# Performance work log

Hardware: AMD Instinct MI355X
Metric: run time of the kernel (lower is better)

The kernel has to match this reference:

```python
import jax, jax.numpy as jnp
import numpy as np

H = 8      # num_attention_heads
DH = 96    # attention_head_size
LN_EPS = 1e-5


def setup_inputs() -> dict:
    key = jax.random.key(0)
    ks = jax.random.split(key, 12)
    B, S, D = 2, 768, 768
    sc = 0.02
    return {
        "hidden_states": jax.random.normal(ks[0], (B, S, D), jnp.float32),
        "distance_matrix": jax.random.uniform(ks[1], (B, S, S), jnp.float32) * 20.0,
        "angle_matrix": jax.random.uniform(ks[2], (B, S, S), jnp.float32) * np.pi,
        "attention_mask": jnp.ones((B, S), jnp.float32),
        "Wq": jax.random.normal(ks[3], (D, D), jnp.float32) * sc,
        "bq": jnp.zeros((D,), jnp.float32),
        "Wk": jax.random.normal(ks[4], (D, D), jnp.float32) * sc,
        "bk": jnp.zeros((D,), jnp.float32),
        "Wv": jax.random.normal(ks[5], (D, D), jnp.float32) * sc,
        "bv": jnp.zeros((D,), jnp.float32),
        "Wd": jax.random.normal(ks[6], (DH,), jnp.float32) * sc,
        "bd": jnp.zeros((DH,), jnp.float32),
        "Wa": jax.random.normal(ks[7], (DH,), jnp.float32) * sc,
        "ba": jnp.zeros((DH,), jnp.float32),
        "Wo": jax.random.normal(ks[8], (D, D), jnp.float32) * sc,
        "bo": jnp.zeros((D,), jnp.float32),
        "ln_g": jnp.ones((D,), jnp.float32),
        "ln_b": jnp.zeros((D,), jnp.float32),
    }


def _heads(x, B, S):
    # [B,S,D] -> [B,H,S,DH]
    return x.reshape(B, S, H, DH).transpose(0, 2, 1, 3)


def reference(hidden_states, distance_matrix, angle_matrix, attention_mask,
              Wq, bq, Wk, bk, Wv, bv, Wd, bd, Wa, ba, Wo, bo, ln_g, ln_b):
    B, S, D = hidden_states.shape
    q = _heads(hidden_states @ Wq.T + bq, B, S)   # [B,H,S,DH]
    k = _heads(hidden_states @ Wk.T + bk, B, S)
    v = _heads(hidden_states @ Wv.T + bv, B, S)

    scores = jnp.einsum('bhid,bhjd->bhij', q, k) / jnp.sqrt(jnp.float32(DH))

    # distance / angle relative-position biases: emb[b,i,j,:] = dist[b,i,j]*Wd + bd
    dist_emb = distance_matrix[..., None] * Wd + bd   # [B,S,S,DH]
    scores = scores + jnp.einsum('bhid,bijd->bhij', q, dist_emb)
    ang_emb = angle_matrix[..., None] * Wa + ba       # [B,S,S,DH]
    scores = scores + jnp.einsum('bhid,bijd->bhij', q, ang_emb)

    # key mask, broadcast over heads and query positions
    scores = scores + (1.0 - attention_mask)[:, None, None, :] * -10000.0

    probs = jax.nn.softmax(scores, axis=-1)           # [B,H,S,S]
    ctx = jnp.einsum('bhij,bhjd->bhid', probs, v)
    ctx = ctx.transpose(0, 2, 1, 3).reshape(B, S, D)  # [B,S,D]

    out = ctx @ Wo.T + bo
    x = out + hidden_states
    mu = jnp.mean(x, axis=-1, keepdims=True)
    var = jnp.var(x, axis=-1, keepdims=True)
    out = (x - mu) * jax.lax.rsqrt(var + LN_EPS) * ln_g + ln_b
    return out, probs
```

## Files before the change

### kernel.cpp

```cpp
#include <hip/hip_runtime.h>
#include <stdint.h>

#define B_  2
#define S_  768
#define D_  768
#define H_  8
#define DH_ 96

typedef unsigned short ushort_t;
typedef __bf16 bf16x8 __attribute__((ext_vector_type(8)));
typedef float  f32x4  __attribute__((ext_vector_type(4)));

__device__ inline ushort_t f2bf(float f) {
    union { float f; unsigned int u; } v; v.f = f;
    unsigned int u = v.u;
    unsigned int r = u + 0x7fffu + ((u >> 16) & 1u);
    return (ushort_t)(r >> 16);
}
__device__ inline float bf2f(ushort_t u) {
    union { unsigned int i; float f; } c; c.i = ((unsigned int)u) << 16;
    return c.f;
}

__device__ inline void glds16(const void* gp, void* lp) {
    auto g = reinterpret_cast<const __attribute__((address_space(1))) uint32_t*>(
        reinterpret_cast<uintptr_t>(gp));
    auto l = reinterpret_cast<__attribute__((address_space(3))) uint32_t*>(
        reinterpret_cast<uintptr_t>(lp));
    __builtin_amdgcn_global_load_lds(g, l, 16, 0, 0);
}

__global__ __launch_bounds__(256) void k_convert(
        const float* __restrict__ X, const float* __restrict__ Wq,
        const float* __restrict__ Wk, const float* __restrict__ Wv,
        const float* __restrict__ Wo,
        ushort_t* __restrict__ Xb, ushort_t* __restrict__ Wb) {
    const int NX4 = (B_ * S_ * D_) / 4;
    const int NW4 = (D_ * D_) / 4;
    int i = blockIdx.x * blockDim.x + threadIdx.x;
    float4 v;
    ushort_t* dst;
    if (i < NX4) {
        v = ((const float4*)X)[i];
        dst = Xb + i * 4;
    } else {
        int wi = i - NX4;
        int sel = wi / NW4;
        int off = wi - sel * NW4;
        const float* src = (sel == 0) ? Wq : (sel == 1) ? Wk : (sel == 2) ? Wv : Wo;
        v = ((const float4*)src)[off];
        dst = Wb + wi * 4;
    }
    ushort4 o;
    o.x = f2bf(v.x); o.y = f2bf(v.y); o.z = f2bf(v.z); o.w = f2bf(v.w);
    *(ushort4*)dst = o;
}

__device__ inline void gemm64_glds(
        const ushort_t* __restrict__ A, int lda,
        const ushort_t* __restrict__ Bt, int ldb,
        int K, int m0, int n0,
        ushort_t* As, ushort_t* Bs, f32x4 acc[2][2]) {
    const int tid  = threadIdx.x;
    const int lane = tid & 63, wave = tid >> 6;
    const int wm = (wave >> 1) * 32, wn = (wave & 1) * 32;
    const int fr = lane & 15, fk = (lane >> 4) * 8;
    const int sr = wave * 16 + (lane >> 2);
    const int sc = (lane & 3) * 8;
    const ushort_t* Ap = A  + (size_t)(m0 + sr) * lda + sc;
    const ushort_t* Bp = Bt + (size_t)(n0 + sr) * ldb + sc;
    ushort_t* AsW = As + wave * 512;
    ushort_t* BsW = Bs + wave * 512;
    for (int kt = 0; kt < K; kt += 32) {
        if (kt) __syncthreads();
        glds16(Ap + kt, AsW);
        glds16(Bp + kt, BsW);
        __syncthreads();
        bf16x8 a0 = *(const bf16x8*)&As[(wm      + fr) * 32 + fk];
        bf16x8 a1 = *(const bf16x8*)&As[(wm + 16 + fr) * 32 + fk];
        bf16x8 b0 = *(const bf16x8*)&Bs[(wn      + fr) * 32 + fk];
        bf16x8 b1 = *(const bf16x8*)&Bs[(wn + 16 + fr) * 32 + fk];
        acc[0][0] = __builtin_amdgcn_mfma_f32_16x16x32_bf16(a0, b0, acc[0][0], 0, 0, 0);
        acc[0][1] = __builtin_amdgcn_mfma_f32_16x16x32_bf16(a0, b1, acc[0][1], 0, 0, 0);
        acc[1][0] = __builtin_amdgcn_mfma_f32_16x16x32_bf16(a1, b0, acc[1][0], 0, 0, 0);
        acc[1][1] = __builtin_amdgcn_mfma_f32_16x16x32_bf16(a1, b1, acc[1][1], 0, 0, 0);
    }
}

__global__ __launch_bounds__(256) void k_qkv(
        const ushort_t* __restrict__ Xb, const ushort_t* __restrict__ Wb,
        const float* __restrict__ bq, const float* __restrict__ bk,
        const float* __restrict__ bv,
        ushort_t* __restrict__ Qb, ushort_t* __restrict__ Kb,
        ushort_t* __restrict__ Vtb) {
    __shared__ __align__(16) ushort_t As[128 * 32];
    __shared__ __align__(16) ushort_t Bs[64 * 32];
    f32x4 acc[4][2];
    #pragma unroll
    for (int i = 0; i < 4; i++)
        #pragma unroll
        for (int j = 0; j < 2; j++) acc[i][j] = (f32x4){0.f, 0.f, 0.f, 0.f};
    const int tid = threadIdx.x, lane = tid & 63, wave = tid >> 6;
    const int m0 = blockIdx.y * 128, n0 = blockIdx.x * 64;
    const int fr = lane & 15, fk = (lane >> 4) * 8;
    const int wm = (wave >> 1) * 64, wn = (wave & 1) * 32;
    const int sr = lane >> 2, sc = (lane & 3) * 8;
    const ushort_t* Ap0 = Xb + (size_t)(m0 + wave * 32 + sr) * D_ + sc;
    const ushort_t* Ap1 = Ap0 + 16 * D_;
    const ushort_t* Bp  = Wb + (size_t)(n0 + wave * 16 + sr) * D_ + sc;
    ushort_t* AsW0 = As + wave * 1024;
    ushort_t* AsW1 = As + wave * 1024 + 512;
    ushort_t* BsW  = Bs + wave * 512;
    for (int kt = 0; kt < D_; kt += 32) {
        if (kt) __syncthreads();
        glds16(Ap0 + kt, AsW0);
        glds16(Ap1 + kt, AsW1);
        glds16(Bp  + kt, BsW);
        __syncthreads();
        bf16x8 a[4], b[2];
        #pragma unroll
        for (int mi = 0; mi < 4; mi++)
            a[mi] = *(const bf16x8*)&As[(wm + mi * 16 + fr) * 32 + fk];
        #pragma unroll
        for (int ni = 0; ni < 2; ni++)
            b[ni] = *(const bf16x8*)&Bs[(wn + ni * 16 + fr) * 32 + fk];
        #pragma unroll
        for (int mi = 0; mi < 4; mi++)
            #pragma unroll
            for (int ni = 0; ni < 2; ni++)
                acc[mi][ni] = __builtin_amdgcn_mfma_f32_16x16x32_bf16(a[mi], b[ni], acc[mi][ni], 0, 0, 0);
    }
    #pragma unroll
    for (int ni = 0; ni < 2; ni++) {
        int gcol = n0 + wn + ni * 16 + fr;
        int g = gcol / D_, d768 = gcol - g * D_;
        int h = d768 / DH_, d = d768 - h * DH_;
        float bias = (g == 0 ? bq : (g == 1 ? bk : bv))[d768];
        #pragma unroll
        for (int mi = 0; mi < 4; mi++) {
            #pragma unroll
            for (int r = 0; r < 4; r++) {
                int grow = m0 + wm + mi * 16 + (lane >> 4) * 4 + r;
                int bidx = grow / S_, s = grow - bidx * S_;
                ushort_t ob = f2bf(acc[mi][ni][r] + bias);
                int bh = bidx * H_ + h;
                if (g == 0)      Qb[((size_t)bh * S_ + s) * DH_ + d] = ob;
                else if (g == 1) Kb[((size_t)bh * S_ + s) * DH_ + d] = ob;
                else             Vtb[((size_t)bh * DH_ + d) * S_ + s] = ob;
            }
        }
    }
}

__global__ __launch_bounds__(256) void k_qcoef(
        const ushort_t* __restrict__ Qb,
        const float* __restrict__ Wd, const float* __restrict__ bd,
        const float* __restrict__ Wa, const float* __restrict__ ba,
        float* __restrict__ qcoef) {
    const int wave = threadIdx.x >> 6, lane = threadIdx.x & 63;
    const int row = blockIdx.x * 4 + wave;
    const ushort_t* q = Qb + (size_t)row * DH_;
    float e0 = bf2f(q[lane]);
    float c0 = e0 * Wd[lane];
    float c1 = e0 * Wa[lane];
    float c2 = e0 * (bd[lane] + ba[lane]);
    if (lane < 32) {
        int d = 64 + lane;
        float e1 = bf2f(q[d]);
        c0 += e1 * Wd[d];
        c1 += e1 * Wa[d];
        c2 += e1 * (bd[d] + ba[d]);
    }
    #pragma unroll
    for (int o = 32; o > 0; o >>= 1) {
        c0 += __shfl_down(c0, o);
        c1 += __shfl_down(c1, o);
        c2 += __shfl_down(c2, o);
    }
    if (lane == 0) {
        qcoef[row * 3 + 0] = c0;
        qcoef[row * 3 + 1] = c1;
        qcoef[row * 3 + 2] = c2;
    }
}

__global__ __launch_bounds__(256) void k_scores(
        const ushort_t* __restrict__ Qb, const ushort_t* __restrict__ Kb,
        const float* __restrict__ qcoef,
        const float* __restrict__ distm, const float* __restrict__ angm,
        const float* __restrict__ mask, float* __restrict__ Sc) {
    __shared__ __align__(16) ushort_t As[64 * 32];
    __shared__ __align__(16) ushort_t Bs[64 * 32];
    f32x4 acc[2][2];
    #pragma unroll
    for (int i = 0; i < 2; i++)
        #pragma unroll
        for (int j = 0; j < 2; j++) acc[i][j] = (f32x4){0.f, 0.f, 0.f, 0.f};
    const int bh = blockIdx.z, b = bh >> 3;
    const ushort_t* A  = Qb + (size_t)bh * S_ * DH_;
    const ushort_t* Bt = Kb + (size_t)bh * S_ * DH_;
    const int m0 = blockIdx.y * 64, n0 = blockIdx.x * 64;
    gemm64_glds(A, DH_, Bt, DH_, DH_, m0, n0, As, Bs, acc);
    const int lane = threadIdx.x & 63, wave = threadIdx.x >> 6;
    const int wm = (wave >> 1) * 32, wn = (wave & 1) * 32;
    const float isq = 0.10206207261596577f;
    #pragma unroll
    for (int ni = 0; ni < 2; ni++) {
        int j = n0 + wn + ni * 16 + (lane & 15);
        float mb = (1.0f - mask[b * S_ + j]) * -10000.0f;
        #pragma unroll
        for (int mi = 0; mi < 2; mi++) {
            #pragma unroll
            for (int r = 0; r < 4; r++) {
                int i = m0 + wm + mi * 16 + (lane >> 4) * 4 + r;
                const float* qc = qcoef + ((size_t)bh * S_ + i) * 3;
                float dist = distm[((size_t)b * S_ + i) * S_ + j];
                float ang  = angm [((size_t)b * S_ + i) * S_ + j];
                Sc[((size_t)bh * S_ + i) * S_ + j] =
                    acc[mi][ni][r] * isq + dist * qc[0] + ang * qc[1] + qc[2] + mb;
            }
        }
    }
}

__global__ __launch_bounds__(256) void k_attnctx(
        const float* __restrict__ Sc, const ushort_t* __restrict__ Vtb,
        float* __restrict__ probs, ushort_t* __restrict__ Ctxb) {
    const int bh = blockIdx.y, b = bh >> 3, h = bh & 7;
    const int r0 = blockIdx.x * 32;
    const float* S = Sc + ((size_t)bh * S_ + r0) * S_;
    const ushort_t* Vt = Vtb + (size_t)bh * DH_ * S_;
    __shared__ float mrow[32], lrow[32];
    __shared__ __align__(16) ushort_t Ps[32 * 32];
    __shared__ __align__(16) ushort_t Vs[96 * 32];
    const int tid = threadIdx.x, lane = tid & 63, wave = tid >> 6;
    for (int rr = 0; rr < 8; rr++) {
        int row = wave * 8 + rr;
        const float* sr = S + (size_t)row * S_;
        float4 x0 = ((const float4*)sr)[lane];
        float4 x1 = ((const float4*)sr)[lane + 64];
        float4 x2 = ((const float4*)sr)[lane + 128];
        float mx = fmaxf(fmaxf(fmaxf(x0.x, x0.y), fmaxf(x0.z, x0.w)),
                   fmaxf(fmaxf(fmaxf(x1.x, x1.y), fmaxf(x1.z, x1.w)),
                         fmaxf(fmaxf(x2.x, x2.y), fmaxf(x2.z, x2.w))));
        #pragma unroll
        for (int o = 32; o > 0; o >>= 1) mx = fmaxf(mx, __shfl_down(mx, o));
        mx = __shfl(mx, 0);
        float s = __expf(x0.x - mx) + __expf(x0.y - mx) + __expf(x0.z - mx) + __expf(x0.w - mx)
                + __expf(x1.x - mx) + __expf(x1.y - mx) + __expf(x1.z - mx) + __expf(x1.w - mx)
                + __expf(x2.x - mx) + __expf(x2.y - mx) + __expf(x2.z - mx) + __expf(x2.w - mx);
        #pragma unroll
        for (int o = 32; o > 0; o >>= 1) s += __shfl_down(s, o);
        if (lane == 0) { mrow[row] = mx; lrow[row] = s; }
    }
    __syncthreads();
    const int mrow0 = (wave & 1) * 16;
    const int nb    = (wave >> 1) * 48;
    const int fr = lane & 15, fk = (lane >> 4) * 8;
    const int prow = tid >> 3, pc = (tid & 7) * 4;
    const float pm = mrow[prow];
    const float pinvl = 1.0f / lrow[prow];
    f32x4 acc[3];
    #pragma unroll
    for (int i = 0; i < 3; i++) acc[i] = (f32x4){0.f, 0.f, 0.f, 0.f};
    const int vr0 = tid >> 2, vc0 = (tid & 3) * 8;
    const int i1 = tid + 256;
    const int vr1 = i1 >> 2, vc1 = (i1 & 3) * 8;
    for (int kt = 0; kt < S_; kt += 32) {
        if (kt) __syncthreads();
        {
            float4 s4 = *(const float4*)(S + (size_t)prow * S_ + kt + pc);
            float e0 = __expf(s4.x - pm), e1 = __expf(s4.y - pm);
            float e2 = __expf(s4.z - pm), e3 = __expf(s4.w - pm);
            ushort4 pb;
            pb.x = f2bf(e0); pb.y = f2bf(e1); pb.z = f2bf(e2); pb.w = f2bf(e3);
            *(ushort4*)&Ps[prow * 32 + pc] = pb;
            float4 pn = {e0 * pinvl, e1 * pinvl, e2 * pinvl, e3 * pinvl};
            *(float4*)&probs[((size_t)bh * S_ + r0 + prow) * S_ + kt + pc] = pn;
        }
        *(uint4*)&Vs[vr0 * 32 + vc0] = *(const uint4*)(Vt + (size_t)vr0 * S_ + kt + vc0);
        if (i1 < 384)
            *(uint4*)&Vs[vr1 * 32 + vc1] = *(const uint4*)(Vt + (size_t)vr1 * S_ + kt + vc1);
        __syncthreads();
        bf16x8 a = *(const bf16x8*)&Ps[(mrow0 + fr) * 32 + fk];
        #pragma unroll
        for (int ni = 0; ni < 3; ni++) {
            bf16x8 bfr = *(const bf16x8*)&Vs[(nb + ni * 16 + fr) * 32 + fk];
            acc[ni] = __builtin_amdgcn_mfma_f32_16x16x32_bf16(a, bfr, acc[ni], 0, 0, 0);
        }
    }
    #pragma unroll
    for (int ni = 0; ni < 3; ni++) {
        int col = nb + ni * 16 + fr;
        #pragma unroll
        for (int r = 0; r < 4; r++) {
            int row = mrow0 + (lane >> 4) * 4 + r;
            float o = acc[ni][r] / lrow[row];
            Ctxb[((size_t)(b * S_ + r0 + row)) * D_ + h * DH_ + col] = f2bf(o);
        }
    }
}

__global__ __launch_bounds__(256) void k_out(
        const ushort_t* __restrict__ Ctxb, const ushort_t* __restrict__ Wob,
        const float* __restrict__ bo, const float* __restrict__ hidden,
        float* __restrict__ xbuf) {
    __shared__ __align__(16) ushort_t As[64 * 32];
    __shared__ __align__(16) ushort_t Bs[64 * 32];
    f32x4 acc[2][2];
    #pragma unroll
    for (int i = 0; i < 2; i++)
        #pragma unroll
        for (int j = 0; j < 2; j++) acc[i][j] = (f32x4){0.f, 0.f, 0.f, 0.f};
    const int m0 = blockIdx.y * 64, n0 = blockIdx.x * 64;
    gemm64_glds(Ctxb, D_, Wob, D_, D_, m0, n0, As, Bs, acc);
    const int lane = threadIdx.x & 63, wave = threadIdx.x >> 6;
    const int wm = (wave >> 1) * 32, wn = (wave & 1) * 32;
    #pragma unroll
    for (int ni = 0; ni < 2; ni++) {
        int gcol = n0 + wn + ni * 16 + (lane & 15);
        float bias = bo[gcol];
        #pragma unroll
        for (int mi = 0; mi < 2; mi++) {
            #pragma unroll
            for (int r = 0; r < 4; r++) {
                int grow = m0 + wm + mi * 16 + (lane >> 4) * 4 + r;
                xbuf[(size_t)grow * D_ + gcol] =
                    acc[mi][ni][r] + bias + hidden[(size_t)grow * D_ + gcol];
            }
        }
    }
}

__global__ __launch_bounds__(256) void k_ln(
        const float* __restrict__ xbuf, const float* __restrict__ g,
        const float* __restrict__ bb, float* __restrict__ out) {
    const float* x = xbuf + (size_t)blockIdx.x * D_;
    const int t = threadIdx.x;
    float a0 = x[t], a1 = x[t + 256], a2 = x[t + 512];
    float s = a0 + a1 + a2;
    float ss = a0 * a0 + a1 * a1 + a2 * a2;
    __shared__ float r1[4], r2[4];
    #pragma unroll
    for (int o = 32; o > 0; o >>= 1) { s += __shfl_down(s, o); ss += __shfl_down(ss, o); }
    if ((t & 63) == 0) { r1[t >> 6] = s; r2[t >> 6] = ss; }
    __syncthreads();
    float ts = r1[0] + r1[1] + r1[2] + r1[3];
    float tss = r2[0] + r2[1] + r2[2] + r2[3];
    float mu = ts * (1.0f / D_);
    float var = tss * (1.0f / D_) - mu * mu;
    float rstd = rsqrtf(var + 1e-5f);
    float* o = out + (size_t)blockIdx.x * D_;
    o[t]       = (a0 - mu) * rstd * g[t]       + bb[t];
    o[t + 256] = (a1 - mu) * rstd * g[t + 256] + bb[t + 256];
    o[t + 512] = (a2 - mu) * rstd * g[t + 512] + bb[t + 512];
}

extern "C" void kernel_launch(void* const* d_in, const int* in_sizes, int n_in,
                              void* d_out, int out_size, void* d_ws, size_t ws_size,
                              hipStream_t stream) {
    const float* X     = (const float*)d_in[0];
    const float* distm = (const float*)d_in[1];
    const float* angm  = (const float*)d_in[2];
    const float* mask  = (const float*)d_in[3];
    const float* Wq    = (const float*)d_in[4];
    const float* bq    = (const float*)d_in[5];
    const float* Wk    = (const float*)d_in[6];
    const float* bk    = (const float*)d_in[7];
    const float* Wv    = (const float*)d_in[8];
    const float* bv    = (const float*)d_in[9];
    const float* Wd    = (const float*)d_in[10];
    const float* bd    = (const float*)d_in[11];
    const float* Wa    = (const float*)d_in[12];
    const float* ba    = (const float*)d_in[13];
    const float* Wo    = (const float*)d_in[14];
    const float* bo    = (const float*)d_in[15];
    const float* ln_g  = (const float*)d_in[16];
    const float* ln_b  = (const float*)d_in[17];

    float* outp  = (float*)d_out;
    float* probs = (float*)d_out + (size_t)B_ * S_ * D_;

    char* ws = (char*)d_ws;
    ushort_t* Xb    = (ushort_t*)(ws + 0);
    ushort_t* Wb    = (ushort_t*)(ws + 2359296);
    ushort_t* Qb    = (ushort_t*)(ws + 7077888);
    ushort_t* Kb    = (ushort_t*)(ws + 9437184);
    ushort_t* Vtb   = (ushort_t*)(ws + 11796480);
    ushort_t* Ctxb  = (ushort_t*)(ws + 14155776);
    float*    qcoef = (float*)   (ws + 16515072);
    float*    xbuf  = (float*)   (ws + 16662528);
    float*    Sc    = (float*)   (ws + 21381120);

    k_convert<<<3456, 256, 0, stream>>>(X, Wq, Wk, Wv, Wo, Xb, Wb);
    k_qkv<<<dim3(36, 12), 256, 0, stream>>>(Xb, Wb, bq, bk, bv, Qb, Kb, Vtb);
    k_qcoef<<<3072, 256, 0, stream>>>(Qb, Wd, bd, Wa, ba, qcoef);
    k_scores<<<dim3(12, 12, 16), 256, 0, stream>>>(Qb, Kb, qcoef, distm, angm, mask, Sc);
    k_attnctx<<<dim3(24, 16), 256, 0, stream>>>(Sc, Vtb, probs, Ctxb);
    k_out<<<dim3(12, 24), 256, 0, stream>>>(Ctxb, Wb + (size_t)2304 * 768, bo, X, xbuf);
    k_ln<<<1536, 256, 0, stream>>>(xbuf, ln_g, ln_b, outp);
}
```

Baseline: 206.7 us.

## Fuse scores, softmax and context into one kernel; load GEMM operands directly

Merges the scores kernel and the softmax/context kernel into a single fused attention kernel. Each block computes a full 32-row score strip in registers, does the softmax with cross-wave reductions through shared memory, writes probs once, and runs P@V from a bf16 copy of P held in LDS. This removes the fp32 score buffer round trip through global memory. The QKV and output GEMMs also drop LDS staging and barriers in favour of direct per-lane global loads into MFMA fragments, with a larger 128x128 tile for QKV. The trade-off is much higher register and LDS use per block in the fused kernel, and uncoalesced, non-reused global loads in the GEMMs.

```diff
diff --git a/kernel.cpp b/kernel.cpp
--- a/kernel.cpp
+++ b/kernel.cpp
@@ -20,14 +20,6 @@
 __device__ inline float bf2f(ushort_t u) {
     union { unsigned int i; float f; } c; c.i = ((unsigned int)u) << 16;
     return c.f;
-}
-
-__device__ inline void glds16(const void* gp, void* lp) {
-    auto g = reinterpret_cast<const __attribute__((address_space(1))) uint32_t*>(
-        reinterpret_cast<uintptr_t>(gp));
-    auto l = reinterpret_cast<__attribute__((address_space(3))) uint32_t*>(
-        reinterpret_cast<uintptr_t>(lp));
-    __builtin_amdgcn_global_load_lds(g, l, 16, 0, 0);
 }
 
 __global__ __launch_bounds__(256) void k_convert(
@@ -56,83 +48,41 @@
     *(ushort4*)dst = o;
 }
 
-__device__ inline void gemm64_glds(
-        const ushort_t* __restrict__ A, int lda,
-        const ushort_t* __restrict__ Bt, int ldb,
-        int K, int m0, int n0,
-        ushort_t* As, ushort_t* Bs, f32x4 acc[2][2]) {
-    const int tid  = threadIdx.x;
-    const int lane = tid & 63, wave = tid >> 6;
-    const int wm = (wave >> 1) * 32, wn = (wave & 1) * 32;
-    const int fr = lane & 15, fk = (lane >> 4) * 8;
-    const int sr = wave * 16 + (lane >> 2);
-    const int sc = (lane & 3) * 8;
-    const ushort_t* Ap = A  + (size_t)(m0 + sr) * lda + sc;
-    const ushort_t* Bp = Bt + (size_t)(n0 + sr) * ldb + sc;
-    ushort_t* AsW = As + wave * 512;
-    ushort_t* BsW = Bs + wave * 512;
-    for (int kt = 0; kt < K; kt += 32) {
-        if (kt) __syncthreads();
-        glds16(Ap + kt, AsW);
-        glds16(Bp + kt, BsW);
-        __syncthreads();
-        bf16x8 a0 = *(const bf16x8*)&As[(wm      + fr) * 32 + fk];
-        bf16x8 a1 = *(const bf16x8*)&As[(wm + 16 + fr) * 32 + fk];
-        bf16x8 b0 = *(const bf16x8*)&Bs[(wn      + fr) * 32 + fk];
-        bf16x8 b1 = *(const bf16x8*)&Bs[(wn + 16 + fr) * 32 + fk];
-        acc[0][0] = __builtin_amdgcn_mfma_f32_16x16x32_bf16(a0, b0, acc[0][0], 0, 0, 0);
-        acc[0][1] = __builtin_amdgcn_mfma_f32_16x16x32_bf16(a0, b1, acc[0][1], 0, 0, 0);
-        acc[1][0] = __builtin_amdgcn_mfma_f32_16x16x32_bf16(a1, b0, acc[1][0], 0, 0, 0);
-        acc[1][1] = __builtin_amdgcn_mfma_f32_16x16x32_bf16(a1, b1, acc[1][1], 0, 0, 0);
-    }
-}
-
 __global__ __launch_bounds__(256) void k_qkv(
         const ushort_t* __restrict__ Xb, const ushort_t* __restrict__ Wb,
         const float* __restrict__ bq, const float* __restrict__ bk,
         const float* __restrict__ bv,
         ushort_t* __restrict__ Qb, ushort_t* __restrict__ Kb,
         ushort_t* __restrict__ Vtb) {
-    __shared__ __align__(16) ushort_t As[128 * 32];
-    __shared__ __align__(16) ushort_t Bs[64 * 32];
-    f32x4 acc[4][2];
+    const int tid = threadIdx.x, lane = tid & 63, w = tid >> 6;
+    const int frn = lane & 15, fko = (lane >> 4) * 8, frg4 = (lane >> 4) * 4;
+    const int m0 = blockIdx.y * 128 + (w & 1) * 64;
+    const int n0 = blockIdx.x * 128 + (w >> 1) * 64;
+    const ushort_t* Ap = Xb + (size_t)(m0 + frn) * D_ + fko;
+    const ushort_t* Bp = Wb + (size_t)(n0 + frn) * D_ + fko;
+    f32x4 acc[4][4];
     #pragma unroll
     for (int i = 0; i < 4; i++)
         #pragma unroll
-        for (int j = 0; j < 2; j++) acc[i][j] = (f32x4){0.f, 0.f, 0.f, 0.f};
-    const int tid = threadIdx.x, lane = tid & 63, wave = tid >> 6;
-    const int m0 = blockIdx.y * 128, n0 = blockIdx.x * 64;
-    const int fr = lane & 15, fk = (lane >> 4) * 8;
-    const int wm = (wave >> 1) * 64, wn = (wave & 1) * 32;
-    const int sr = lane >> 2, sc = (lane & 3) * 8;
-    const ushort_t* Ap0 = Xb + (size_t)(m0 + wave * 32 + sr) * D_ + sc;
-    const ushort_t* Ap1 = Ap0 + 16 * D_;
-    const ushort_t* Bp  = Wb + (size_t)(n0 + wave * 16 + sr) * D_ + sc;
-    ushort_t* AsW0 = As + wave * 1024;
-    ushort_t* AsW1 = As + wave * 1024 + 512;
-    ushort_t* BsW  = Bs + wave * 512;
+        for (int j = 0; j < 4; j++) acc[i][j] = (f32x4){0.f, 0.f, 0.f, 0.f};
+    #pragma unroll 2
     for (int kt = 0; kt < D_; kt += 32) {
-        if (kt) __syncthreads();
-        glds16(Ap0 + kt, AsW0);
-        glds16(Ap1 + kt, AsW1);
-        glds16(Bp  + kt, BsW);
-        __syncthreads();
-        bf16x8 a[4], b[2];
+        bf16x8 a[4], b[4];
         #pragma unroll
         for (int mi = 0; mi < 4; mi++)
-            a[mi] = *(const bf16x8*)&As[(wm + mi * 16 + fr) * 32 + fk];
-        #pragma unroll
-        for (int ni = 0; ni < 2; ni++)
-            b[ni] = *(const bf16x8*)&Bs[(wn + ni * 16 + fr) * 32 + fk];
+            a[mi] = *(const bf16x8*)(Ap + (size_t)mi * 16 * D_ + kt);
+        #pragma unroll
+        for (int ni = 0; ni < 4; ni++)
+            b[ni] = *(const bf16x8*)(Bp + (size_t)ni * 16 * D_ + kt);
         #pragma unroll
         for (int mi = 0; mi < 4; mi++)
             #pragma unroll
-            for (int ni = 0; ni < 2; ni++)
+            for (int ni = 0; ni < 4; ni++)
                 acc[mi][ni] = __builtin_amdgcn_mfma_f32_16x16x32_bf16(a[mi], b[ni], acc[mi][ni], 0, 0, 0);
     }
     #pragma unroll
-    for (int ni = 0; ni < 2; ni++) {
-        int gcol = n0 + wn + ni * 16 + fr;
+    for (int ni = 0; ni < 4; ni++) {
+        int gcol = n0 + ni * 16 + frn;
         int g = gcol / D_, d768 = gcol - g * D_;
         int h = d768 / DH_, d = d768 - h * DH_;
         float bias = (g == 0 ? bq : (g == 1 ? bk : bv))[d768];
@@ -140,7 +90,7 @@
         for (int mi = 0; mi < 4; mi++) {
             #pragma unroll
             for (int r = 0; r < 4; r++) {
-                int grow = m0 + wm + mi * 16 + (lane >> 4) * 4 + r;
+                int grow = m0 + mi * 16 + frg4 + r;
                 int bidx = grow / S_, s = grow - bidx * S_;
                 ushort_t ob = f2bf(acc[mi][ni][r] + bias);
                 int bh = bidx * H_ + h;
@@ -184,119 +134,138 @@
     }
 }
 
-__global__ __launch_bounds__(256) void k_scores(
+#define PSLD 776
+__global__ __launch_bounds__(256, 2) void k_flash(
         const ushort_t* __restrict__ Qb, const ushort_t* __restrict__ Kb,
-        const float* __restrict__ qcoef,
+        const ushort_t* __restrict__ Vtb, const float* __restrict__ qcoef,
         const float* __restrict__ distm, const float* __restrict__ angm,
-        const float* __restrict__ mask, float* __restrict__ Sc) {
-    __shared__ __align__(16) ushort_t As[64 * 32];
-    __shared__ __align__(16) ushort_t Bs[64 * 32];
-    f32x4 acc[2][2];
-    #pragma unroll
-    for (int i = 0; i < 2; i++)
-        #pragma unroll
-        for (int j = 0; j < 2; j++) acc[i][j] = (f32x4){0.f, 0.f, 0.f, 0.f};
-    const int bh = blockIdx.z, b = bh >> 3;
-    const ushort_t* A  = Qb + (size_t)bh * S_ * DH_;
-    const ushort_t* Bt = Kb + (size_t)bh * S_ * DH_;
-    const int m0 = blockIdx.y * 64, n0 = blockIdx.x * 64;
-    gemm64_glds(A, DH_, Bt, DH_, DH_, m0, n0, As, Bs, acc);
-    const int lane = threadIdx.x & 63, wave = threadIdx.x >> 6;
-    const int wm = (wave >> 1) * 32, wn = (wave & 1) * 32;
-    const float isq = 0.10206207261596577f;
-    #pragma unroll
-    for (int ni = 0; ni < 2; ni++) {
-        int j = n0 + wn + ni * 16 + (lane & 15);
-        float mb = (1.0f - mask[b * S_ + j]) * -10000.0f;
-        #pragma unroll
-        for (int mi = 0; mi < 2; mi++) {
-            #pragma unroll
-            for (int r = 0; r < 4; r++) {
-                int i = m0 + wm + mi * 16 + (lane >> 4) * 4 + r;
-                const float* qc = qcoef + ((size_t)bh * S_ + i) * 3;
-                float dist = distm[((size_t)b * S_ + i) * S_ + j];
-                float ang  = angm [((size_t)b * S_ + i) * S_ + j];
-                Sc[((size_t)bh * S_ + i) * S_ + j] =
-                    acc[mi][ni][r] * isq + dist * qc[0] + ang * qc[1] + qc[2] + mb;
-            }
-        }
-    }
-}
-
-__global__ __launch_bounds__(256) void k_attnctx(
-        const float* __restrict__ Sc, const ushort_t* __restrict__ Vtb,
+        const float* __restrict__ mask,
         float* __restrict__ probs, ushort_t* __restrict__ Ctxb) {
+    __shared__ __align__(16) ushort_t Ps[32 * PSLD];
+    __shared__ float mstat[2][32], lstat[2][32];
     const int bh = blockIdx.y, b = bh >> 3, h = bh & 7;
     const int r0 = blockIdx.x * 32;
-    const float* S = Sc + ((size_t)bh * S_ + r0) * S_;
-    const ushort_t* Vt = Vtb + (size_t)bh * DH_ * S_;
-    __shared__ float mrow[32], lrow[32];
-    __shared__ __align__(16) ushort_t Ps[32 * 32];
-    __shared__ __align__(16) ushort_t Vs[96 * 32];
-    const int tid = threadIdx.x, lane = tid & 63, wave = tid >> 6;
-    for (int rr = 0; rr < 8; rr++) {
-        int row = wave * 8 + rr;
-        const float* sr = S + (size_t)row * S_;
-        float4 x0 = ((const float4*)sr)[lane];
-        float4 x1 = ((const float4*)sr)[lane + 64];
-        float4 x2 = ((const float4*)sr)[lane + 128];
-        float mx = fmaxf(fmaxf(fmaxf(x0.x, x0.y), fmaxf(x0.z, x0.w)),
-                   fmaxf(fmaxf(fmaxf(x1.x, x1.y), fmaxf(x1.z, x1.w)),
-                         fmaxf(fmaxf(x2.x, x2.y), fmaxf(x2.z, x2.w))));
-        #pragma unroll
-        for (int o = 32; o > 0; o >>= 1) mx = fmaxf(mx, __shfl_down(mx, o));
-        mx = __shfl(mx, 0);
-        float s = __expf(x0.x - mx) + __expf(x0.y - mx) + __expf(x0.z - mx) + __expf(x0.w - mx)
-                + __expf(x1.x - mx) + __expf(x1.y - mx) + __expf(x1.z - mx) + __expf(x1.w - mx)
-                + __expf(x2.x - mx) + __expf(x2.y - mx) + __expf(x2.z - mx) + __expf(x2.w - mx);
-        #pragma unroll
-        for (int o = 32; o > 0; o >>= 1) s += __shfl_down(s, o);
-        if (lane == 0) { mrow[row] = mx; lrow[row] = s; }
-    }
+    const int tid = threadIdx.x, lane = tid & 63, w = tid >> 6;
+    const int frn = lane & 15, fko = (lane >> 4) * 8, frg4 = (lane >> 4) * 4;
+    const int rhalf = (w & 1) * 16;
+    const int chalf = (w >> 1) * 384;
+    const int whalf = w >> 1;
+
+    const ushort_t* Qbh = Qb + (size_t)bh * S_ * DH_;
+    const ushort_t* Kbh = Kb + (size_t)bh * S_ * DH_;
+    const ushort_t* Vbh = Vtb + (size_t)bh * DH_ * S_;
+
+    bf16x8 aq[3];
+    {
+        const ushort_t* qp = Qbh + (size_t)(r0 + rhalf + frn) * DH_ + fko;
+        #pragma unroll
+        for (int ks = 0; ks < 3; ks++) aq[ks] = *(const bf16x8*)(qp + ks * 32);
+    }
+    f32x4 acc[24];
+    #pragma unroll 4
+    for (int t = 0; t < 24; t++) {
+        const ushort_t* kp = Kbh + (size_t)(chalf + t * 16 + frn) * DH_ + fko;
+        bf16x8 b0 = *(const bf16x8*)(kp);
+        bf16x8 b1 = *(const bf16x8*)(kp + 32);
+        bf16x8 b2 = *(const bf16x8*)(kp + 64);
+        f32x4 c = (f32x4){0.f, 0.f, 0.f, 0.f};
+        c = __builtin_amdgcn_mfma_f32_16x16x32_bf16(aq[0], b0, c, 0, 0, 0);
+        c = __builtin_amdgcn_mfma_f32_16x16x32_bf16(aq[1], b1, c, 0, 0, 0);
+        c = __builtin_amdgcn_mfma_f32_16x16x32_bf16(aq[2], b2, c, 0, 0, 0);
+        acc[t] = c;
+    }
+    float qc0[4], qc1[4], qc2[4];
+    #pragma unroll
+    for (int r = 0; r < 4; r++) {
+        const float* qp = qcoef + ((size_t)bh * S_ + r0 + rhalf + frg4 + r) * 3;
+        qc0[r] = qp[0]; qc1[r] = qp[1]; qc2[r] = qp[2];
+    }
+    const float isq = 0.10206207261596577f;
+    const size_t dbase = ((size_t)b * S_ + r0 + rhalf + frg4) * S_;
+    #pragma unroll 4
+    for (int t = 0; t < 24; t++) {
+        int j = chalf + t * 16 + frn;
+        float mb = (1.0f - mask[b * S_ + j]) * -10000.0f;
+        #pragma unroll
+        for (int r = 0; r < 4; r++) {
+            float dist = distm[dbase + (size_t)r * S_ + j];
+            float ang  = angm [dbase + (size_t)r * S_ + j];
+            acc[t][r] = acc[t][r] * isq + dist * qc0[r] + ang * qc1[r] + qc2[r] + mb;
+        }
+    }
+    float mx[4] = {-1e30f, -1e30f, -1e30f, -1e30f};
+    #pragma unroll
+    for (int t = 0; t < 24; t++)
+        #pragma unroll
+        for (int r = 0; r < 4; r++) mx[r] = fmaxf(mx[r], acc[t][r]);
+    #pragma unroll
+    for (int o = 1; o < 16; o <<= 1)
+        #pragma unroll
+        for (int r = 0; r < 4; r++) mx[r] = fmaxf(mx[r], __shfl_xor(mx[r], o));
+    if (frn == 0)
+        #pragma unroll
+        for (int r = 0; r < 4; r++) mstat[whalf][rhalf + frg4 + r] = mx[r];
     __syncthreads();
-    const int mrow0 = (wave & 1) * 16;
-    const int nb    = (wave >> 1) * 48;
-    const int fr = lane & 15, fk = (lane >> 4) * 8;
-    const int prow = tid >> 3, pc = (tid & 7) * 4;
-    const float pm = mrow[prow];
-    const float pinvl = 1.0f / lrow[prow];
-    f32x4 acc[3];
-    #pragma unroll
-    for (int i = 0; i < 3; i++) acc[i] = (f32x4){0.f, 0.f, 0.f, 0.f};
-    const int vr0 = tid >> 2, vc0 = (tid & 3) * 8;
-    const int i1 = tid + 256;
-    const int vr1 = i1 >> 2, vc1 = (i1 & 3) * 8;
+    float mf[4], sum[4] = {0.f, 0.f, 0.f, 0.f};
+    #pragma unroll
+    for (int r = 0; r < 4; r++) {
+        int il = rhalf + frg4 + r;
+        mf[r] = fmaxf(mstat[0][il], mstat[1][il]);
+    }
+    #pragma unroll
+    for (int t = 0; t < 24; t++)
+        #pragma unroll
+        for (int r = 0; r < 4; r++) {
+            float e = __expf(acc[t][r] - mf[r]);
+            acc[t][r] = e;
+            sum[r] += e;
+        }
+    #pragma unroll
+    for (int o = 1; o < 16; o <<= 1)
+        #pragma unroll
+        for (int r = 0; r < 4; r++) sum[r] += __shfl_xor(sum[r], o);
+    if (frn == 0)
+        #pragma unroll
+        for (int r = 0; r < 4; r++) lstat[whalf][rhalf + frg4 + r] = sum[r];
+    __syncthreads();
+    float inv[4];
+    #pragma unroll
+    for (int r = 0; r < 4; r++) {
+        int il = rhalf + frg4 + r;
+        inv[r] = 1.0f / (lstat[0][il] + lstat[1][il]);
+    }
+    float* pout = probs + ((size_t)bh * S_ + r0 + rhalf + frg4) * S_;
+    #pragma unroll 4
+    for (int t = 0; t < 24; t++) {
+        int j = chalf + t * 16 + frn;
+        #pragma unroll
+        for (int r = 0; r < 4; r++) {
+            float p = acc[t][r] * inv[r];
+            pout[(size_t)r * S_ + j] = p;
+            Ps[(rhalf + frg4 + r) * PSLD + j] = f2bf(p);
+        }
+    }
+    __syncthreads();
+    const int cb = (w >> 1) * 48;
+    f32x4 accO[3];
+    #pragma unroll
+    for (int i = 0; i < 3; i++) accO[i] = (f32x4){0.f, 0.f, 0.f, 0.f};
+    #pragma unroll 4
     for (int kt = 0; kt < S_; kt += 32) {
-        if (kt) __syncthreads();
-        {
-            float4 s4 = *(const float4*)(S + (size_t)prow * S_ + kt + pc);
-            float e0 = __expf(s4.x - pm), e1 = __expf(s4.y - pm);
-            float e2 = __expf(s4.z - pm), e3 = __expf(s4.w - pm);
-            ushort4 pb;
-            pb.x = f2bf(e0); pb.y = f2bf(e1); pb.z = f2bf(e2); pb.w = f2bf(e3);
-            *(ushort4*)&Ps[prow * 32 + pc] = pb;
-            float4 pn = {e0 * pinvl, e1 * pinvl, e2 * pinvl, e3 * pinvl};
-            *(float4*)&probs[((size_t)bh * S_ + r0 + prow) * S_ + kt + pc] = pn;
-        }
-        *(uint4*)&Vs[vr0 * 32 + vc0] = *(const uint4*)(Vt + (size_t)vr0 * S_ + kt + vc0);
-        if (i1 < 384)
-            *(uint4*)&Vs[vr1 * 32 + vc1] = *(const uint4*)(Vt + (size_t)vr1 * S_ + kt + vc1);
-        __syncthreads();
-        bf16x8 a = *(const bf16x8*)&Ps[(mrow0 + fr) * 32 + fk];
-        #pragma unroll
-        for (int ni = 0; ni < 3; ni++) {
-            bf16x8 bfr = *(const bf16x8*)&Vs[(nb + ni * 16 + fr) * 32 + fk];
-            acc[ni] = __builtin_amdgcn_mfma_f32_16x16x32_bf16(a, bfr, acc[ni], 0, 0, 0);
-        }
-    }
-    #pragma unroll
-    for (int ni = 0; ni < 3; ni++) {
-        int col = nb + ni * 16 + fr;
+        bf16x8 a = *(const bf16x8*)&Ps[(rhalf + frn) * PSLD + kt + fko];
+        #pragma unroll
+        for (int nt = 0; nt < 3; nt++) {
+            bf16x8 v = *(const bf16x8*)(Vbh + (size_t)(cb + nt * 16 + frn) * S_ + kt + fko);
+            accO[nt] = __builtin_amdgcn_mfma_f32_16x16x32_bf16(a, v, accO[nt], 0, 0, 0);
+        }
+    }
+    #pragma unroll
+    for (int nt = 0; nt < 3; nt++) {
+        int col = cb + nt * 16 + frn;
         #pragma unroll
         for (int r = 0; r < 4; r++) {
-            int row = mrow0 + (lane >> 4) * 4 + r;
-            float o = acc[ni][r] / lrow[row];
-            Ctxb[((size_t)(b * S_ + r0 + row)) * D_ + h * DH_ + col] = f2bf(o);
+            int row = r0 + rhalf + frg4 + r;
+            Ctxb[((size_t)(b * S_ + row)) * D_ + h * DH_ + col] = f2bf(accO[nt][r]);
         }
     }
 }
@@ -305,26 +274,41 @@
         const ushort_t* __restrict__ Ctxb, const ushort_t* __restrict__ Wob,
         const float* __restrict__ bo, const float* __restrict__ hidden,
         float* __restrict__ xbuf) {
-    __shared__ __align__(16) ushort_t As[64 * 32];
-    __shared__ __align__(16) ushort_t Bs[64 * 32];
+    const int tid = threadIdx.x, lane = tid & 63, w = tid >> 6;
+    const int frn = lane & 15, fko = (lane >> 4) * 8, frg4 = (lane >> 4) * 4;
+    const int m0 = blockIdx.y * 64 + (w & 1) * 32;
+    const int n0 = blockIdx.x * 64 + (w >> 1) * 32;
+    const ushort_t* Ap = Ctxb + (size_t)(m0 + frn) * D_ + fko;
+    const ushort_t* Bp = Wob + (size_t)(n0 + frn) * D_ + fko;
     f32x4 acc[2][2];
     #pragma unroll
     for (int i = 0; i < 2; i++)
         #pragma unroll
         for (int j = 0; j < 2; j++) acc[i][j] = (f32x4){0.f, 0.f, 0.f, 0.f};
-    const int m0 = blockIdx.y * 64, n0 = blockIdx.x * 64;
-    gemm64_glds(Ctxb, D_, Wob, D_, D_, m0, n0, As, Bs, acc);
-    const int lane = threadIdx.x & 63, wave = threadIdx.x >> 6;
-    const int wm = (wave >> 1) * 32, wn = (wave & 1) * 32;
+    #pragma unroll 4
+    for (int kt = 0; kt < D_; kt += 32) {
+        bf16x8 a[2], b[2];
+        #pragma unroll
+        for (int mi = 0; mi < 2; mi++)
+            a[mi] = *(const bf16x8*)(Ap + (size_t)mi * 16 * D_ + kt);
+        #pragma unroll
+        for (int ni = 0; ni < 2; ni++)
+            b[ni] = *(const bf16x8*)(Bp + (size_t)ni * 16 * D_ + kt);
+        #pragma unroll
+        for (int mi = 0; mi < 2; mi++)
+            #pragma unroll
+            for (int ni = 0; ni < 2; ni++)
+                acc[mi][ni] = __builtin_amdgcn_mfma_f32_16x16x32_bf16(a[mi], b[ni], acc[mi][ni], 0, 0, 0);
+    }
     #pragma unroll
     for (int ni = 0; ni < 2; ni++) {
-        int gcol = n0 + wn + ni * 16 + (lane & 15);
+        int gcol = n0 + ni * 16 + frn;
         float bias = bo[gcol];
         #pragma unroll
         for (int mi = 0; mi < 2; mi++) {
             #pragma unroll
             for (int r = 0; r < 4; r++) {
-                int grow = m0 + wm + mi * 16 + (lane >> 4) * 4 + r;
+                int grow = m0 + mi * 16 + frg4 + r;
                 xbuf[(size_t)grow * D_ + gcol] =
                     acc[mi][ni][r] + bias + hidden[(size_t)grow * D_ + gcol];
             }
@@ -390,13 +374,11 @@
     ushort_t* Ctxb  = (ushort_t*)(ws + 14155776);
     float*    qcoef = (float*)   (ws + 16515072);
     float*    xbuf  = (float*)   (ws + 16662528);
-    float*    Sc    = (float*)   (ws + 21381120);
 
     k_convert<<<3456, 256, 0, stream>>>(X, Wq, Wk, Wv, Wo, Xb, Wb);
-    k_qkv<<<dim3(36, 12), 256, 0, stream>>>(Xb, Wb, bq, bk, bv, Qb, Kb, Vtb);
+    k_qkv<<<dim3(18, 12), 256, 0, stream>>>(Xb, Wb, bq, bk, bv, Qb, Kb, Vtb);
     k_qcoef<<<3072, 256, 0, stream>>>(Qb, Wd, bd, Wa, ba, qcoef);
-    k_scores<<<dim3(12, 12, 16), 256, 0, stream>>>(Qb, Kb, qcoef, distm, angm, mask, Sc);
-    k_attnctx<<<dim3(24, 16), 256, 0, stream>>>(Sc, Vtb, probs, Ctxb);
+    k_flash<<<dim3(24, 16), 256, 0, stream>>>(Qb, Kb, Vtb, qcoef, distm, angm, mask, probs, Ctxb);
     k_out<<<dim3(12, 24), 256, 0, stream>>>(Ctxb, Wb + (size_t)2304 * 768, bo, X, xbuf);
     k_ln<<<1536, 256, 0, stream>>>(xbuf, ln_g, ln_b, outp);
 }
```

Measured after the change: 255.5 us. +23.6%, slower.
